# Kernel optimization log

Measured on AMD Instinct MI355X. Metric: run time of the kernel, lower is better.

Reference implementation:

```python
import jax, jax.numpy as jnp
import numpy as np
import math

FREQ_DIM = 161
OUTPUT_DIM = 4096
RNN_DIM = 128
EMBED_DIM = 32


def conv2d(x, w, b, stride):
    # x: (B, Cin, H, W), w: (Cout, Cin, kh, kw)
    out = jax.lax.conv_general_dilated(x, w, window_strides=stride, padding='VALID',
                                       dimension_numbers=('NCHW', 'OIHW', 'NCHW'))
    return out + b[None, :, None, None]


def gru_seq(x, w_ih, w_hh, b_ih, b_hh, h0):
    # x: (B, T, D); PyTorch GRU gate order: r, z, n
    B, T, D = x.shape
    H = h0.shape[-1]
    xg = jnp.einsum('btd,gd->btg', x, w_ih) + b_ih  # (B, T, 3H)

    def step(h, xg_t):
        hg = h @ w_hh.T + b_hh
        xr, xz, xn = jnp.split(xg_t, 3, axis=-1)
        hr, hz, hn = jnp.split(hg, 3, axis=-1)
        r = jax.nn.sigmoid(xr + hr)
        z = jax.nn.sigmoid(xz + hz)
        n = jnp.tanh(xn + r * hn)
        h_new = (1 - z) * n + z * h
        return h_new, h_new

    _, hs = jax.lax.scan(step, h0, jnp.swapaxes(xg, 0, 1))
    return jnp.swapaxes(hs, 0, 1)  # (B, T, H)


def gru_cell(ix, h, w_ih, w_hh, b_ih, b_hh):
    xg = ix @ w_ih.T + b_ih
    hg = h @ w_hh.T + b_hh
    xr, xz, xn = jnp.split(xg, 3, axis=-1)
    hr, hz, hn = jnp.split(hg, 3, axis=-1)
    r = jax.nn.sigmoid(xr + hr)
    z = jax.nn.sigmoid(xz + hz)
    n = jnp.tanh(xn + r * hn)
    return (1 - z) * n + z * h


def attend(eh, dhx):
    # eh: (B, T, H), dhx: (B, H)
    scores = jnp.einsum('bth,bh->bt', eh, dhx)
    a = jax.nn.softmax(scores, axis=-1)
    return jnp.einsum('bth,bt->bh', eh, a)


def setup_inputs() -> dict:
    key = jax.random.key(0)
    ks = jax.random.split(key, 16)

    def rn(k, shape, fan_in):
        s = 1.0 / math.sqrt(fan_in)
        return jax.random.uniform(k, shape, jnp.float32, -s, s)

    B, T_audio, L = 32, 512, 128
    x = jax.random.normal(ks[0], (B, T_audio, FREQ_DIM), jnp.float32)
    y = jax.random.randint(ks[1], (B, L), 0, OUTPUT_DIM)

    conv_in = 544  # 17 * 32 after two convs on freq dim 161
    params = {
        'conv1_w': rn(ks[2], (32, 1, 5, 32), 1 * 5 * 32),
        'conv1_b': rn(ks[3], (32,), 1 * 5 * 32),
        'conv2_w': rn(ks[4], (32, 32, 5, 32), 32 * 5 * 32),
        'conv2_b': rn(ks[5], (32,), 32 * 5 * 32),
        'rnn_w_ih': rn(ks[6], (3 * RNN_DIM, conv_in), RNN_DIM),
        'rnn_w_hh': rn(ks[7], (3 * RNN_DIM, RNN_DIM), RNN_DIM),
        'rnn_b_ih': rn(ks[8], (3 * RNN_DIM,), RNN_DIM),
        'rnn_b_hh': rn(ks[9], (3 * RNN_DIM,), RNN_DIM),
        'emb': jax.random.normal(ks[10], (OUTPUT_DIM, EMBED_DIM), jnp.float32),
        'dec_w_ih': rn(ks[11], (3 * RNN_DIM, EMBED_DIM), RNN_DIM),
        'dec_w_hh': rn(ks[12], (3 * RNN_DIM, RNN_DIM), RNN_DIM),
        'dec_b_ih': rn(ks[13], (3 * RNN_DIM,), RNN_DIM),
        'dec_b_hh': rn(ks[14], (3 * RNN_DIM,), RNN_DIM),
        'fc_w': rn(ks[15], (OUTPUT_DIM, RNN_DIM), RNN_DIM),
        'fc_b': rn(jax.random.fold_in(key, 99), (OUTPUT_DIM,), RNN_DIM),
        'h_init': jnp.zeros((1, RNN_DIM), jnp.float32),
    }
    return {'x': x, 'y': y, **params}


def forward(x, y, conv1_w, conv1_b, conv2_w, conv2_b,
            rnn_w_ih, rnn_w_hh, rnn_b_ih, rnn_b_hh,
            emb, dec_w_ih, dec_w_hh, dec_b_ih, dec_b_hh,
            fc_w, fc_b, h_init):
    B = x.shape[0]
    h = x[:, None, :, :]  # (B, 1, T, F)
    h = jax.nn.relu(conv2d(h, conv1_w, conv1_b, (2, 2)))
    h = jax.nn.relu(conv2d(h, conv2_w, conv2_b, (2, 2)))  # (B, 32, t, f)
    h = jnp.transpose(h, (0, 2, 3, 1))  # (B, t, f, c)
    b, t, f, c = h.shape
    h = h.reshape(b, t, f * c)
    eh = gru_seq(h, rnn_w_ih, rnn_w_hh, rnn_b_ih, rnn_b_hh,
                 jnp.zeros((b, RNN_DIM), h.dtype))  # (B, t, 128)

    inputs = emb[y[:, :-1]]  # (B, L-1, 32)
    hx = jnp.broadcast_to(h_init, (B, RNN_DIM))
    hx = hx + attend(eh, hx)

    def step(hx, ix):
        hx = gru_cell(ix, hx, dec_w_ih, dec_w_hh, dec_b_ih, dec_b_hh)
        hx = hx + attend(eh, hx)
        return hx, hx

    _, outs = jax.lax.scan(step, hx, jnp.swapaxes(inputs, 0, 1))
    out = jnp.concatenate([hx[:, None, :], jnp.swapaxes(outs, 0, 1)], axis=1)  # (B, L, 128)
    logits = jnp.einsum('btd,od->bto', out, fc_w) + fc_b
    return logits


def reference(x, y, conv1_w, conv1_b, conv2_w, conv2_b,
              rnn_w_ih, rnn_w_hh, rnn_b_ih, rnn_b_hh,
              emb, dec_w_ih, dec_w_hh, dec_b_ih, dec_b_hh,
              fc_w, fc_b, h_init):
    return forward(x, y, conv1_w, conv1_b, conv2_w, conv2_b,
                   rnn_w_ih, rnn_w_hh, rnn_b_ih, rnn_b_hh,
                   emb, dec_w_ih, dec_w_hh, dec_b_ih, dec_b_hh,
                   fc_w, fc_b, h_init)
```

## Files before the change

### kernel.cpp

```cpp
#include <hip/hip_runtime.h>
#include <stdint.h>

typedef unsigned short u16;
typedef uint32_t u32;

typedef __bf16 bf16x8 __attribute__((ext_vector_type(8)));
typedef float f32x4 __attribute__((ext_vector_type(4)));
typedef _Float16 h2v __attribute__((ext_vector_type(2)));

union B8 { uint4 q; u32 u[4]; bf16x8 v; };

__device__ __forceinline__ u16 f2bf(float f) {
  u32 u = __float_as_uint(f);
  u32 r = (u + 0x7fffu + ((u >> 16) & 1u)) >> 16;
  return (u16)r;
}
__device__ __forceinline__ u16 f2h(float f) {
  union { _Float16 h; u16 u; } v; v.h = (_Float16)f; return v.u;
}
__device__ __forceinline__ float dot2h(u32 a, u32 b, float c) {
  union U { u32 u; h2v v; } A, B; A.u = a; B.u = b;
  return __builtin_amdgcn_fdot2(A.v, B.v, c, false);
}
__device__ __forceinline__ float sigf(float x) { return 1.f / (1.f + __expf(-x)); }
__device__ __forceinline__ float tanhf_fast(float x) {
  x = fminf(fmaxf(x, -15.f), 15.f);
  float e = __expf(2.f * x);
  return (e - 1.f) / (e + 1.f);
}

__device__ __forceinline__ void prep_one(int e,
    const float* rnn_w_hh, const float* dec_w_hh, const float* conv1_w,
    const float* conv2_w, const float* rnn_w_ih, const float* dec_w_ih,
    const float* fc_w, const float* emb, const int* y,
    u32* wT2e, u32* wT2d, u16* w1b, u16* w2b, u16* wihb, u16* dwihb,
    u16* fcwb, u16* adec)
{
  const int S0 = 24576, S1 = 24576, S2 = 5120, S3 = 163840, S4 = 208896,
            S5 = 12288, S6 = 524288, S7 = 130048;
  if (e < S0) { int g = e >> 6, k2 = e & 63;
    wT2e[e] = (u32)f2h(rnn_w_hh[g*128 + 2*k2]) | ((u32)f2h(rnn_w_hh[g*128 + 2*k2 + 1]) << 16);
    return; }
  e -= S0;
  if (e < S1) { int g = e >> 6, k2 = e & 63;
    wT2d[e] = (u32)f2h(dec_w_hh[g*128 + 2*k2]) | ((u32)f2h(dec_w_hh[g*128 + 2*k2 + 1]) << 16);
    return; }
  e -= S1;
  if (e < S2) { int kh = e >> 10, c = (e >> 5) & 31, kw = e & 31;
    w1b[e] = f2bf(conv1_w[c*160 + kh*32 + kw]); return; }
  e -= S2;
  if (e < S3) { int kt = e >> 10, c = (e >> 5) & 31, kw = e & 31;
    int ic = kt / 5, kh = kt - ic * 5;
    w2b[e] = f2bf(conv2_w[((c*32 + ic)*5 + kh)*32 + kw]); return; }
  e -= S3;
  if (e < S4) { wihb[e] = f2bf(rnn_w_ih[e]); return; }
  e -= S4;
  if (e < S5) { dwihb[e] = f2bf(dec_w_ih[e]); return; }
  e -= S5;
  if (e < S6) { fcwb[e] = f2bf(fc_w[e]); return; }
  e -= S6;
  if (e < S7) { int m = e >> 5, k = e & 31;
    int b = m / 127, t = m - b * 127;
    adec[e] = f2bf(emb[y[b*128 + t]*32 + k]); return; }
}

__global__ __launch_bounds__(256) void prep_k(
    const float* rnn_w_hh, const float* dec_w_hh, const float* conv1_w,
    const float* conv2_w, const float* rnn_w_ih, const float* dec_w_ih,
    const float* fc_w, const float* emb, const int* y,
    u32* wT2e, u32* wT2d, u16* w1b, u16* w2b, u16* wihb, u16* dwihb,
    u16* fcwb, u16* adec)
{
  int e0 = blockIdx.x * 256 + threadIdx.x;
  #pragma unroll
  for (int it = 0; it < 4; it++) {
    int e = e0 + it * 273408;
    if (e < 1093632)
      prep_one(e, rnn_w_hh, dec_w_hh, conv1_w, conv2_w, rnn_w_ih, dec_w_ih,
               fc_w, emb, y, wT2e, wT2d, w1b, w2b, wihb, dwihb, fcwb, adec);
  }
}

__global__ __launch_bounds__(256) void conv1_k(const float* x, const u16* w1b,
                                               const float* c1b, u16* in1b)
{
  __shared__ __align__(16) u16 slab[35 * 162];
  __shared__ __align__(16) u16 wl[5120];
  int b = blockIdx.x >> 4;
  int oh0 = (blockIdx.x & 15) * 16;
  int ih0 = oh0 * 2;
  for (int e = threadIdx.x; e < 35 * 161; e += 256) {
    int r = e / 161, iw = e - r * 161;
    int ih = ih0 + r;
    float v = (ih < 512) ? x[(b*512 + ih)*161 + iw] : 0.f;
    slab[r*162 + iw] = f2bf(v);
  }
  for (int e = threadIdx.x; e < 5120; e += 256) wl[e] = w1b[e];
  __syncthreads();
  int lane = threadIdx.x & 63, wid = threadIdx.x >> 6;
  int lrow = lane & 15, lk = (lane >> 4) * 8;
  B8 bw[5][2];
  #pragma unroll
  for (int kt = 0; kt < 5; kt++)
    #pragma unroll
    for (int ct = 0; ct < 2; ct++)
      bw[kt][ct].q = *(const uint4*)&wl[(kt*32 + ct*16 + lrow)*32 + lk];
  float bias0 = c1b[lrow], bias1 = c1b[16 + lrow];
  for (int mt = wid; mt < 65; mt += 4) {
    int m = mt * 16 + lrow;
    int ohl = m / 65, ow = m - ohl * 65;
    int ro = ohl * 324 + ow * 2 + lk;
    f32x4 a0, a1;
    #pragma unroll
    for (int i = 0; i < 4; i++) { a0[i] = 0.f; a1[i] = 0.f; }
    #pragma unroll
    for (int kt = 0; kt < 5; kt++) {
      B8 af;
      const u32* p = (const u32*)&slab[ro + kt * 162];
      af.u[0] = p[0]; af.u[1] = p[1]; af.u[2] = p[2]; af.u[3] = p[3];
      a0 = __builtin_amdgcn_mfma_f32_16x16x32_bf16(af.v, bw[kt][0].v, a0, 0, 0, 0);
      a1 = __builtin_amdgcn_mfma_f32_16x16x32_bf16(af.v, bw[kt][1].v, a1, 0, 0, 0);
    }
    int rb = mt * 16 + (lane >> 4) * 4;
    #pragma unroll
    for (int i = 0; i < 4; i++) {
      int mr = rb + i;
      int ohl2 = mr / 65, ow2 = mr - ohl2 * 65;
      int oh = oh0 + ohl2;
      if (oh < 254) {
        float v0 = fmaxf(a0[i] + bias0, 0.f);
        float v1 = fmaxf(a1[i] + bias1, 0.f);
        in1b[((b*32 + lrow)*254 + oh)*72 + ow2] = f2bf(v0);
        in1b[((b*32 + 16 + lrow)*254 + oh)*72 + ow2] = f2bf(v1);
      }
    }
  }
}

__global__ __launch_bounds__(256) void conv2_k(const u16* in1b, const u16* w2b,
                                               const float* c2b, u16* hbf)
{
  extern __shared__ char smem[];
  u16* slab = (u16*)smem;
  u16* wl = (u16*)(smem + 50688);
  int b = blockIdx.x >> 5;
  int tile = blockIdx.x & 31;
  int oh0 = tile * 4;
  int ih0 = oh0 * 2;
  for (int q = threadIdx.x; q < 3168; q += 256) {
    int ic = q / 99;
    int rem = q - ic * 99;
    int r = rem / 9, j = rem - r * 9;
    int ih = ih0 + r;
    uint4 v = make_uint4(0u, 0u, 0u, 0u);
    if (ih < 254) v = *(const uint4*)&in1b[(((b*32 + ic)*254 + ih)*72) + j*8];
    *(uint4*)&slab[(ic*11 + r)*72 + j*8] = v;
  }
  int lane = threadIdx.x & 63, wid = threadIdx.x >> 6;
  int lrow = lane & 15, lk = (lane >> 4) * 8;
  int ohl_[2], ow_[2];
  #pragma unroll
  for (int q = 0; q < 2; q++) {
    int mt = (q == 1) ? 4 : wid;
    int m = mt * 16 + lrow;
    if (m > 67) m = 0;
    ohl_[q] = m / 17; ow_[q] = m - ohl_[q] * 17;
  }
  f32x4 acc[2][2];
  #pragma unroll
  for (int q = 0; q < 2; q++)
    #pragma unroll
    for (int ct = 0; ct < 2; ct++)
      #pragma unroll
      for (int i = 0; i < 4; i++) acc[q][ct][i] = 0.f;

  for (int ph = 0; ph < 16; ph++) {
    __syncthreads();
    {
      const uint4* s4 = (const uint4*)&w2b[ph * 10240];
      uint4* d4 = (uint4*)wl;
      for (int q = threadIdx.x; q < 1280; q += 256) d4[q] = s4[q];
    }
    __syncthreads();
    for (int ktl = 0; ktl < 10; ktl++) {
      int ktg = ph * 10 + ktl;
      int ic = ktg / 5, kh = ktg - ic * 5;
      B8 fb0, fb1;
      fb0.q = *(const uint4*)&wl[(ktl*32 + lrow)*32 + lk];
      fb1.q = *(const uint4*)&wl[(ktl*32 + 16 + lrow)*32 + lk];
      int base = (ic * 11 + kh) * 72 + lk;
      #pragma unroll
      for (int q = 0; q < 2; q++) {
        if (q == 1 && wid != 0) break;
        B8 af;
        const u32* p = (const u32*)&slab[base + ohl_[q] * 144 + ow_[q] * 2];
        af.u[0] = p[0]; af.u[1] = p[1]; af.u[2] = p[2]; af.u[3] = p[3];
        acc[q][0] = __builtin_amdgcn_mfma_f32_16x16x32_bf16(af.v, fb0.v, acc[q][0], 0, 0, 0);
        acc[q][1] = __builtin_amdgcn_mfma_f32_16x16x32_bf16(af.v, fb1.v, acc[q][1], 0, 0, 0);
      }
    }
  }
  #pragma unroll
  for (int q = 0; q < 2; q++) {
    if (q == 1 && wid != 0) break;
    int mt = (q == 1) ? 4 : wid;
    int rb = mt * 16 + (lane >> 4) * 4;
    #pragma unroll
    for (int ct = 0; ct < 2; ct++) {
      int c = ct * 16 + lrow;
      float bias = c2b[c];
      #pragma unroll
      for (int i = 0; i < 4; i++) {
        int mr = rb + i;
        if (mr < 68) {
          int ohl = mr / 17, ow = mr - ohl * 17;
          int oh = oh0 + ohl;
          if (oh < 125) {
            float v = fmaxf(acc[q][ct][i] + bias, 0.f);
            hbf[(b*125 + oh)*544 + ow*32 + c] = f2bf(v);
          }
        }
      }
    }
  }
}

__global__ __launch_bounds__(256) void gemm_k(const u16* A, const u16* Bw,
                                              const float* bias, float* C,
                                              int M, int N, int K)
{
  __shared__ __align__(16) u16 As[64 * 32];
  __shared__ __align__(16) u16 Bs[64 * 32];
  int m0 = blockIdx.x * 64, n0 = blockIdx.y * 64;
  int tid = threadIdx.x;
  int lane = tid & 63, wid = tid >> 6;
  int lrow = lane & 15, lk = (lane >> 4) * 8;
  int sr = tid >> 2, sc8 = (tid & 3) * 8;
  f32x4 acc[4];
  #pragma unroll
  for (int nt = 0; nt < 4; nt++)
    #pragma unroll
    for (int i = 0; i < 4; i++) acc[nt][i] = 0.f;
  int nkt = K >> 5;
  for (int kt = 0; kt < nkt; kt++) {
    __syncthreads();
    uint4 va = make_uint4(0u, 0u, 0u, 0u);
    int arow = m0 + sr;
    if (arow < M) va = *(const uint4*)&A[arow * K + kt * 32 + sc8];
    *(uint4*)&As[sr * 32 + sc8] = va;
    uint4 vb = *(const uint4*)&Bw[(n0 + sr) * K + kt * 32 + sc8];
    *(uint4*)&Bs[sr * 32 + sc8] = vb;
    __syncthreads();
    B8 af; af.q = *(const uint4*)&As[(wid * 16 + lrow) * 32 + lk];
    #pragma unroll
    for (int nt = 0; nt < 4; nt++) {
      B8 bb; bb.q = *(const uint4*)&Bs[(nt * 16 + lrow) * 32 + lk];
      acc[nt] = __builtin_amdgcn_mfma_f32_16x16x32_bf16(af.v, bb.v, acc[nt], 0, 0, 0);
    }
  }
  #pragma unroll
  for (int nt = 0; nt < 4; nt++) {
    int col = n0 + nt * 16 + lrow;
    float bv = bias[col];
    #pragma unroll
    for (int i = 0; i < 4; i++) {
      int row = m0 + wid * 16 + (lane >> 4) * 4 + i;
      if (row < M) C[row * N + col] = acc[nt][i] + bv;
    }
  }
}

__global__ __launch_bounds__(256) void fc_k(const u16* A, const u16* Bw,
                                            const float* bias, float* C)
{
  __shared__ __align__(16) u16 As[128 * 32];
  __shared__ __align__(16) u16 Bs[64 * 32];
  int m0 = blockIdx.x * 128, n0 = blockIdx.y * 64;
  int tid = threadIdx.x;
  int lane = tid & 63, wid = tid >> 6;
  int lrow = lane & 15, lk = (lane >> 4) * 8;
  f32x4 acc[2][4];
  #pragma unroll
  for (int mq = 0; mq < 2; mq++)
    #pragma unroll
    for (int nt = 0; nt < 4; nt++)
      #pragma unroll
      for (int i = 0; i < 4; i++) acc[mq][nt][i] = 0.f;
  #pragma unroll
  for (int kt = 0; kt < 4; kt++) {
    __syncthreads();
    #pragma unroll
    for (int i = tid; i < 512; i += 256) {
      int row = i >> 2, q = i & 3;
      *(uint4*)&As[row * 32 + q * 8] = *(const uint4*)&A[(m0 + row) * 128 + kt * 32 + q * 8];
    }
    {
      int row = tid >> 2, q = tid & 3;
      *(uint4*)&Bs[row * 32 + q * 8] = *(const uint4*)&Bw[(n0 + row) * 128 + kt * 32 + q * 8];
    }
    __syncthreads();
    B8 bb[4];
    #pragma unroll
    for (int nt = 0; nt < 4; nt++) bb[nt].q = *(const uint4*)&Bs[(nt * 16 + lrow) * 32 + lk];
    #pragma unroll
    for (int mq = 0; mq < 2; mq++) {
      B8 af; af.q = *(const uint4*)&As[((wid * 2 + mq) * 16 + lrow) * 32 + lk];
      #pragma unroll
      for (int nt = 0; nt < 4; nt++)
        acc[mq][nt] = __builtin_amdgcn_mfma_f32_16x16x32_bf16(af.v, bb[nt].v, acc[mq][nt], 0, 0, 0);
    }
  }
  #pragma unroll
  for (int nt = 0; nt < 4; nt++) {
    int col = n0 + nt * 16 + lrow;
    float bv = bias[col];
    #pragma unroll
    for (int mq = 0; mq < 2; mq++)
      #pragma unroll
      for (int i = 0; i < 4; i++) {
        int row = m0 + (wid * 2 + mq) * 16 + (lane >> 4) * 4 + i;
        C[(size_t)row * 4096 + col] = acc[mq][nt][i] + bv;
      }
  }
}

__global__ __launch_bounds__(1024, 1) void enc_k(const u32* wT2, const float* xg,
                                                 const float* bhh_g, u16* ehk, u16* eht)
{
  __shared__ __align__(16) u32 hp[2][2][64];
  __shared__ float hg[2][1152];
  int tid = threadIdx.x;
  int g = tid >> 9, tb = tid & 511, kh = tb >> 7, t = tb & 127;
  int b = blockIdx.x * 2 + g;
  u32 w0[16], w1[16], w2[16];
  {
    const uint4* p0 = (const uint4*)(wT2 + (size_t)t * 64 + kh * 16);
    const uint4* p1 = (const uint4*)(wT2 + (size_t)(128 + t) * 64 + kh * 16);
    const uint4* p2 = (const uint4*)(wT2 + (size_t)(256 + t) * 64 + kh * 16);
    #pragma unroll
    for (int j = 0; j < 4; j++) {
      uint4 q0 = p0[j]; w0[4*j] = q0.x; w0[4*j+1] = q0.y; w0[4*j+2] = q0.z; w0[4*j+3] = q0.w;
      uint4 q1 = p1[j]; w1[4*j] = q1.x; w1[4*j+1] = q1.y; w1[4*j+2] = q1.z; w1[4*j+3] = q1.w;
      uint4 q2 = p2[j]; w2[4*j] = q2.x; w2[4*j+1] = q2.y; w2[4*j+2] = q2.z; w2[4*j+3] = q2.w;
    }
  }
  float b0 = 0.f, b1 = 0.f, b2 = 0.f, xr0 = 0.f, xr1 = 0.f, xr2 = 0.f, hreg = 0.f;
  if (kh == 0) {
    b0 = bhh_g[t]; b1 = bhh_g[128 + t]; b2 = bhh_g[256 + t];
    const float* xp = &xg[(size_t)b * 125 * 384];
    xr0 = xp[t]; xr1 = xp[128 + t]; xr2 = xp[256 + t];
    ((u16*)&hp[g][0][0])[t] = 0;
  }
  __syncthreads();
  for (int tt = 0; tt < 125; tt++) {
    const u32* hb = &hp[g][tt & 1][kh * 16];
    float r0 = 0.f, r1 = 0.f, z0 = 0.f, z1 = 0.f, n0 = 0.f, n1 = 0.f;
    #pragma unroll
    for (int j = 0; j < 4; j++) {
      uint4 hv = *(const uint4*)&hb[4*j];
      r0 = dot2h(w0[4*j+0], hv.x, r0); r1 = dot2h(w0[4*j+1], hv.y, r1);
      r0 = dot2h(w0[4*j+2], hv.z, r0); r1 = dot2h(w0[4*j+3], hv.w, r1);
      z0 = dot2h(w1[4*j+0], hv.x, z0); z1 = dot2h(w1[4*j+1], hv.y, z1);
      z0 = dot2h(w1[4*j+2], hv.z, z0); z1 = dot2h(w1[4*j+3], hv.w, z1);
      n0 = dot2h(w2[4*j+0], hv.x, n0); n1 = dot2h(w2[4*j+1], hv.y, n1);
      n0 = dot2h(w2[4*j+2], hv.z, n0); n1 = dot2h(w2[4*j+3], hv.w, n1);
    }
    if (kh) {
      float* hh = &hg[g][(kh - 1) * 384];
      hh[t] = r0 + r1; hh[128 + t] = z0 + z1; hh[256 + t] = n0 + n1;
    }
    __syncthreads();
    if (kh == 0) {
      const float* hh = &hg[g][0];
      float pr = r0 + r1 + hh[t] + hh[384 + t] + hh[768 + t];
      float pz = z0 + z1 + hh[128 + t] + hh[512 + t] + hh[896 + t];
      float pn = n0 + n1 + hh[256 + t] + hh[640 + t] + hh[1024 + t];
      float r = sigf(xr0 + pr + b0);
      float z = sigf(xr1 + pz + b1);
      float n = tanhf_fast(xr2 + r * (pn + b2));
      hreg = (1.f - z) * n + z * hreg;
      u16 hv = f2h(hreg);
      ((u16*)&hp[g][(tt & 1) ^ 1][0])[t] = hv;
      ehk[((size_t)(b*64 + (t >> 1)) * 125 + tt) * 2 + (t & 1)] = hv;
      eht[((size_t)(b*128 + t)) * 128 + tt] = hv;
      if (tt + 1 < 125) {
        const float* xq = &xg[((size_t)b * 125 + tt + 1) * 384];
        xr0 = xq[t]; xr1 = xq[128 + t]; xr2 = xq[256 + t];
      }
    }
    __syncthreads();
  }
  if (kh == 0) {
    size_t rb = ((size_t)(b*128 + t)) * 128;
    eht[rb + 125] = 0; eht[rb + 126] = 0; eht[rb + 127] = 0;
  }
}

__global__ __launch_bounds__(1024, 1) void dec_k(const u32* wT2, const u32* ehk_g,
                                                 const u32* eht_g, const float* xgd,
                                                 const float* bhh_g, const float* h_init,
                                                 u16* outb)
{
  extern __shared__ char sm[];
  int tid = threadIdx.x;
  int g = tid >> 9, tb = tid & 511, kh = tb >> 7, t = tb & 127;
  int b = blockIdx.x * 2 + g;
  char* base = sm + (size_t)g * 41024;
  u32* elK   = (u32*)base;
  float* hgP = (float*)(base + 32000);
  float* sp  = (float*)(base + 36608);
  float* ctxB= (float*)(base + 38656);
  u16* hxA   = (u16*)(base + 40192);
  u16* hxB   = (u16*)(base + 40448);
  u16* scp   = (u16*)(base + 40704);
  float* red = (float*)(base + 40960);

  u32 w0[16], w1[16], w2[16];
  {
    const uint4* p0 = (const uint4*)(wT2 + (size_t)t * 64 + kh * 16);
    const uint4* p1 = (const uint4*)(wT2 + (size_t)(128 + t) * 64 + kh * 16);
    const uint4* p2 = (const uint4*)(wT2 + (size_t)(256 + t) * 64 + kh * 16);
    #pragma unroll
    for (int j = 0; j < 4; j++) {
      uint4 q0 = p0[j]; w0[4*j] = q0.x; w0[4*j+1] = q0.y; w0[4*j+2] = q0.z; w0[4*j+3] = q0.w;
      uint4 q1 = p1[j]; w1[4*j] = q1.x; w1[4*j+1] = q1.y; w1[4*j+2] = q1.z; w1[4*j+3] = q1.w;
      uint4 q2 = p2[j]; w2[4*j] = q2.x; w2[4*j+1] = q2.y; w2[4*j+2] = q2.z; w2[4*j+3] = q2.w;
    }
  }
  u32 rowr[16];
  {
    const uint4* rp = (const uint4*)(eht_g + (size_t)b * 8192 + (size_t)t * 64 + kh * 16);
    #pragma unroll
    for (int j = 0; j < 4; j++) {
      uint4 q = rp[j]; rowr[4*j] = q.x; rowr[4*j+1] = q.y; rowr[4*j+2] = q.z; rowr[4*j+3] = q.w;
    }
  }
  for (int e = tb; e < 8000; e += 512) elK[e] = ehk_g[(size_t)b * 8000 + e];
  float b0 = 0.f, b1 = 0.f, b2 = 0.f, xr0 = 0.f, xr1 = 0.f, xr2 = 0.f;
  float hxf = 0.f, hxg = 0.f;
  if (kh == 0) {
    b0 = bhh_g[t]; b1 = bhh_g[128 + t]; b2 = bhh_g[256 + t];
    hxf = h_init[t];
    const float* xp = &xgd[(size_t)b * 127 * 384];
    xr0 = xp[t]; xr1 = xp[128 + t]; xr2 = xp[256 + t];
  }
  __syncthreads();

  for (int step = 0; step < 128; step++) {
    if (step > 0) {
      const u32* hb = (const u32*)hxB + kh * 16;
      float r0 = 0.f, r1 = 0.f, z0 = 0.f, z1 = 0.f, n0 = 0.f, n1 = 0.f;
      #pragma unroll
      for (int j = 0; j < 4; j++) {
        uint4 hv = *(const uint4*)&hb[4*j];
        r0 = dot2h(w0[4*j+0], hv.x, r0); r1 = dot2h(w0[4*j+1], hv.y, r1);
        r0 = dot2h(w0[4*j+2], hv.z, r0); r1 = dot2h(w0[4*j+3], hv.w, r1);
        z0 = dot2h(w1[4*j+0], hv.x, z0); z1 = dot2h(w1[4*j+1], hv.y, z1);
        z0 = dot2h(w1[4*j+2], hv.z, z0); z1 = dot2h(w1[4*j+3], hv.w, z1);
        n0 = dot2h(w2[4*j+0], hv.x, n0); n1 = dot2h(w2[4*j+1], hv.y, n1);
        n0 = dot2h(w2[4*j+2], hv.z, n0); n1 = dot2h(w2[4*j+3], hv.w, n1);
      }
      if (kh) {
        float* hh = &hgP[(kh - 1) * 384];
        hh[t] = r0 + r1; hh[128 + t] = z0 + z1; hh[256 + t] = n0 + n1;
      }
      __syncthreads();
      if (kh == 0) {
        float pr = r0 + r1 + hgP[t] + hgP[384 + t] + hgP[768 + t];
        float pz = z0 + z1 + hgP[128 + t] + hgP[512 + t] + hgP[896 + t];
        float pn = n0 + n1 + hgP[256 + t] + hgP[640 + t] + hgP[1024 + t];
        float r = sigf(xr0 + pr + b0);
        float z = sigf(xr1 + pz + b1);
        float n = tanhf_fast(xr2 + r * (pn + b2));
        hxg = (1.f - z) * n + z * hxf;
        ((u16*)hxA)[t] = f2h(hxg);
        if (step < 127) {
          const float* xq = &xgd[((size_t)b * 127 + step) * 384];
          xr0 = xq[t]; xr1 = xq[128 + t]; xr2 = xq[256 + t];
        }
      }
      __syncthreads();
    } else {
      if (kh == 0) { hxg = hxf; ((u16*)hxA)[t] = f2h(hxg); }
      __syncthreads();
    }
    {
      float s0 = 0.f, s1 = 0.f;
      const u32* ek = &elK[(kh * 16) * 125];
      const u32* hxA4 = (const u32*)hxA;
      #pragma unroll
      for (int j = 0; j < 4; j++) {
        uint4 aw = *(const uint4*)&hxA4[kh * 16 + 4*j];
        s0 = dot2h(ek[(4*j+0)*125 + t], aw.x, s0);
        s1 = dot2h(ek[(4*j+1)*125 + t], aw.y, s1);
        s0 = dot2h(ek[(4*j+2)*125 + t], aw.z, s0);
        s1 = dot2h(ek[(4*j+3)*125 + t], aw.w, s1);
      }
      sp[kh * 128 + t] = s0 + s1;
    }
    __syncthreads();
    if (kh == 0) {
      float s = (t < 125) ? (sp[t] + sp[128 + t] + sp[256 + t] + sp[384 + t]) : -1e30f;
      float mw = s;
      #pragma unroll
      for (int o = 32; o > 0; o >>= 1) mw = fmaxf(mw, __shfl_xor(mw, o));
      float ev = (t < 125) ? __expf(s - mw) : 0.f;
      float sw = ev;
      #pragma unroll
      for (int o = 32; o > 0; o >>= 1) sw += __shfl_xor(sw, o);
      ((u16*)scp)[t] = f2h(ev);
      if ((t & 63) == 0) { int wv = t >> 6; red[wv*2] = mw; red[wv*2 + 1] = sw; }
    }
    __syncthreads();
    float m0r = red[0], S0r = red[1], m1r = red[2], S1r = red[3];
    float M = fmaxf(m0r, m1r);
    float f0 = __expf(m0r - M), f1 = __expf(m1r - M);
    float inv = 1.f / (f0 * S0r + f1 * S1r);
    float c0 = 0.f, c1 = 0.f;
    {
      const u32* scp4 = (const u32*)scp;
      #pragma unroll
      for (int j = 0; j < 4; j++) {
        uint4 sw4 = *(const uint4*)&scp4[kh * 16 + 4*j];
        c0 = dot2h(rowr[4*j+0], sw4.x, c0); c1 = dot2h(rowr[4*j+1], sw4.y, c1);
        c0 = dot2h(rowr[4*j+2], sw4.z, c0); c1 = dot2h(rowr[4*j+3], sw4.w, c1);
      }
    }
    if (kh) ctxB[(kh - 1) * 128 + t] = c0 + c1;
    __syncthreads();
    if (kh == 0) {
      float ctx = ((c0 + c1) + ctxB[t]) * f0 + (ctxB[128 + t] + ctxB[256 + t]) * f1;
      hxf = hxg + ctx * inv;
      outb[((size_t)(b * 128) + step) * 128 + t] = f2bf(hxf);
      ((u16*)hxB)[t] = f2h(hxf);
    }
    __syncthreads();
  }
}

extern "C" void kernel_launch(void* const* d_in, const int* in_sizes, int n_in,
                              void* d_out, int out_size, void* d_ws, size_t ws_size,
                              hipStream_t stream)
{
  const float* x        = (const float*)d_in[0];
  const int*   y        = (const int*)d_in[1];
  const float* conv1_w  = (const float*)d_in[2];
  const float* conv1_b  = (const float*)d_in[3];
  const float* conv2_w  = (const float*)d_in[4];
  const float* conv2_b  = (const float*)d_in[5];
  const float* rnn_w_ih = (const float*)d_in[6];
  const float* rnn_w_hh = (const float*)d_in[7];
  const float* rnn_b_ih = (const float*)d_in[8];
  const float* rnn_b_hh = (const float*)d_in[9];
  const float* emb      = (const float*)d_in[10];
  const float* dec_w_ih = (const float*)d_in[11];
  const float* dec_w_hh = (const float*)d_in[12];
  const float* dec_b_ih = (const float*)d_in[13];
  const float* dec_b_hh = (const float*)d_in[14];
  const float* fc_w     = (const float*)d_in[15];
  const float* fc_b     = (const float*)d_in[16];
  const float* h_init   = (const float*)d_in[17];
  float* logits = (float*)d_out;

  char* ws = (char*)d_ws;
  size_t off = 0;
  auto alloc = [&](size_t bytes) { char* p = ws + off; off = (off + bytes + 255) & ~(size_t)255; return p; };
  u16* in1b  = (u16*)alloc(37453824);
  u16* hbf   = (u16*)alloc(4352000);
  float* xge = (float*)alloc(6144000);
  u32* ehb_k = (u32*)alloc(1024000);
  u32* ehb_t = (u32*)alloc(1048576);
  float* xgd = (float*)alloc(6242304);
  u16* adec  = (u16*)alloc(260096);
  u16* outb  = (u16*)alloc(1048576);
  u32* wT2e  = (u32*)alloc(98304);
  u32* wT2d  = (u32*)alloc(98304);
  u16* w1b   = (u16*)alloc(10240);
  u16* w2b   = (u16*)alloc(327680);
  u16* wihb  = (u16*)alloc(417792);
  u16* dwihb = (u16*)alloc(24576);
  u16* fcwb  = (u16*)alloc(1048576);

  hipFuncSetAttribute((const void*)conv2_k, hipFuncAttributeMaxDynamicSharedMemorySize, 71168);
  hipFuncSetAttribute((const void*)dec_k,   hipFuncAttributeMaxDynamicSharedMemorySize, 82048);

  prep_k<<<1068, 256, 0, stream>>>(rnn_w_hh, dec_w_hh, conv1_w, conv2_w, rnn_w_ih,
                                   dec_w_ih, fc_w, emb, y,
                                   wT2e, wT2d, w1b, w2b, wihb, dwihb, fcwb, adec);
  conv1_k<<<512, 256, 0, stream>>>(x, w1b, conv1_b, in1b);
  conv2_k<<<1024, 256, 71168, stream>>>(in1b, w2b, conv2_b, hbf);
  gemm_k<<<dim3(63, 6), 256, 0, stream>>>(hbf, wihb, rnn_b_ih, xge, 4000, 384, 544);
  gemm_k<<<dim3(64, 6), 256, 0, stream>>>(adec, dwihb, dec_b_ih, xgd, 4064, 384, 32);
  enc_k<<<16, 1024, 0, stream>>>(wT2e, xge, rnn_b_hh, (u16*)ehb_k, (u16*)ehb_t);
  dec_k<<<16, 1024, 82048, stream>>>(wT2d, ehb_k, ehb_t, xgd, dec_b_hh, h_init, outb);
  fc_k<<<dim3(32, 64), 256, 0, stream>>>(outb, fcwb, fc_b, logits);
}
```

Measured before the change: 601.7 us.

## Stage recurrent input gates and outputs in LDS in 8-step chunks

In the encoder and decoder recurrent kernels, input-gate projections are now bulk-loaded into shared memory every 8 timesteps by all threads, replacing per-step scalar global loads on the critical path. Hidden-state outputs are likewise buffered in shared memory and written out as coalesced 32-bit chunks every 8 steps, replacing scattered 16-bit stores. The aim is to take global memory latency off the serial recurrence. In exchange the kernels use more shared memory, and every eighth step carries a burst of global traffic.

```diff
diff --git a/kernel.cpp b/kernel.cpp
--- a/kernel.cpp
+++ b/kernel.cpp
@@ -325,13 +325,16 @@
 }
 
 __global__ __launch_bounds__(1024, 1) void enc_k(const u32* wT2, const float* xg,
-                                                 const float* bhh_g, u16* ehk, u16* eht)
+                                                 const float* bhh_g, u32* ehk, u32* eht)
 {
   __shared__ __align__(16) u32 hp[2][2][64];
   __shared__ float hg[2][1152];
+  __shared__ __align__(16) float xgL[2][3072];
+  __shared__ __align__(16) u32 ehkC[2][512];
+  __shared__ __align__(16) u32 ehtC[2][512];
   int tid = threadIdx.x;
   int g = tid >> 9, tb = tid & 511, kh = tb >> 7, t = tb & 127;
-  int b = blockIdx.x * 2 + g;
+  int bg = blockIdx.x * 2 + g;
   u32 w0[16], w1[16], w2[16];
   {
     const uint4* p0 = (const uint4*)(wT2 + (size_t)t * 64 + kh * 16);
@@ -344,15 +347,29 @@
       uint4 q2 = p2[j]; w2[4*j] = q2.x; w2[4*j+1] = q2.y; w2[4*j+2] = q2.z; w2[4*j+3] = q2.w;
     }
   }
-  float b0 = 0.f, b1 = 0.f, b2 = 0.f, xr0 = 0.f, xr1 = 0.f, xr2 = 0.f, hreg = 0.f;
+  float b0 = 0.f, b1 = 0.f, b2 = 0.f, hreg = 0.f;
   if (kh == 0) {
     b0 = bhh_g[t]; b1 = bhh_g[128 + t]; b2 = bhh_g[256 + t];
-    const float* xp = &xg[(size_t)b * 125 * 384];
-    xr0 = xp[t]; xr1 = xp[128 + t]; xr2 = xp[256 + t];
     ((u16*)&hp[g][0][0])[t] = 0;
   }
   __syncthreads();
   for (int tt = 0; tt < 125; tt++) {
+    if (tt && (tt & 7) == 0) {
+      int tb0 = tt - 8;
+      { int k2 = tb >> 3, i = tb & 7;
+        ehk[(size_t)(bg*64 + k2)*125 + tb0 + i] = ehkC[g][k2*8 + i]; }
+      { int t2 = tb >> 2, i = tb & 3;
+        eht[(size_t)(bg*128 + t2)*64 + (tb0 >> 1) + i] = ehtC[g][t2*4 + i]; }
+    }
+    if ((tt & 7) == 0) {
+      #pragma unroll
+      for (int i = 0; i < 6; i++) {
+        int idx = tb + i * 512;
+        int r = idx / 384, col = idx - r * 384;
+        int gr = tt + r;
+        xgL[g][idx] = (gr < 125) ? xg[((size_t)bg * 125 + gr) * 384 + col] : 0.f;
+      }
+    }
     const u32* hb = &hp[g][tt & 1][kh * 16];
     float r0 = 0.f, r1 = 0.f, z0 = 0.f, z1 = 0.f, n0 = 0.f, n1 = 0.f;
     #pragma unroll
@@ -372,27 +389,31 @@
     __syncthreads();
     if (kh == 0) {
       const float* hh = &hg[g][0];
+      const float* xr = &xgL[g][(tt & 7) * 384];
       float pr = r0 + r1 + hh[t] + hh[384 + t] + hh[768 + t];
       float pz = z0 + z1 + hh[128 + t] + hh[512 + t] + hh[896 + t];
       float pn = n0 + n1 + hh[256 + t] + hh[640 + t] + hh[1024 + t];
-      float r = sigf(xr0 + pr + b0);
-      float z = sigf(xr1 + pz + b1);
-      float n = tanhf_fast(xr2 + r * (pn + b2));
+      float r = sigf(xr[t] + pr + b0);
+      float z = sigf(xr[128 + t] + pz + b1);
+      float n = tanhf_fast(xr[256 + t] + r * (pn + b2));
       hreg = (1.f - z) * n + z * hreg;
       u16 hv = f2h(hreg);
       ((u16*)&hp[g][(tt & 1) ^ 1][0])[t] = hv;
-      ehk[((size_t)(b*64 + (t >> 1)) * 125 + tt) * 2 + (t & 1)] = hv;
-      eht[((size_t)(b*128 + t)) * 128 + tt] = hv;
-      if (tt + 1 < 125) {
-        const float* xq = &xg[((size_t)b * 125 + tt + 1) * 384];
-        xr0 = xq[t]; xr1 = xq[128 + t]; xr2 = xq[256 + t];
-      }
+      ((u16*)&ehkC[g][0])[(t >> 1) * 16 + (tt & 7) * 2 + (t & 1)] = hv;
+      ((u16*)&ehtC[g][0])[t * 8 + (tt & 7)] = hv;
     }
     __syncthreads();
   }
   if (kh == 0) {
-    size_t rb = ((size_t)(b*128 + t)) * 128;
-    eht[rb + 125] = 0; eht[rb + 126] = 0; eht[rb + 127] = 0;
+    u16* ec = (u16*)&ehtC[g][0];
+    ec[t*8 + 5] = 0; ec[t*8 + 6] = 0; ec[t*8 + 7] = 0;
+  }
+  __syncthreads();
+  {
+    { int k2 = tb >> 3, i = tb & 7, ttg = 120 + i;
+      if (ttg < 125) ehk[(size_t)(bg*64 + k2)*125 + ttg] = ehkC[g][k2*8 + i]; }
+    { int t2 = tb >> 2, i = tb & 3;
+      eht[(size_t)(bg*128 + t2)*64 + 60 + i] = ehtC[g][t2*4 + i]; }
   }
 }
 
@@ -405,15 +426,17 @@
   int tid = threadIdx.x;
   int g = tid >> 9, tb = tid & 511, kh = tb >> 7, t = tb & 127;
   int b = blockIdx.x * 2 + g;
-  char* base = sm + (size_t)g * 41024;
-  u32* elK   = (u32*)base;
-  float* hgP = (float*)(base + 32000);
-  float* sp  = (float*)(base + 36608);
-  float* ctxB= (float*)(base + 38656);
-  u16* hxA   = (u16*)(base + 40192);
-  u16* hxB   = (u16*)(base + 40448);
-  u16* scp   = (u16*)(base + 40704);
-  float* red = (float*)(base + 40960);
+  char* base = sm + (size_t)g * 55360;
+  u32* elK    = (u32*)base;
+  float* hgP  = (float*)(base + 32000);
+  float* sp   = (float*)(base + 36608);
+  float* ctxB = (float*)(base + 38656);
+  u16* hxA    = (u16*)(base + 40192);
+  u16* hxB    = (u16*)(base + 40448);
+  u16* scp    = (u16*)(base + 40704);
+  float* red  = (float*)(base + 40960);
+  float* xgdL = (float*)(base + 41024);
+  u32* outbL  = (u32*)(base + 53312);
 
   u32 w0[16], w1[16], w2[16];
   {
@@ -436,17 +459,18 @@
     }
   }
   for (int e = tb; e < 8000; e += 512) elK[e] = ehk_g[(size_t)b * 8000 + e];
-  float b0 = 0.f, b1 = 0.f, b2 = 0.f, xr0 = 0.f, xr1 = 0.f, xr2 = 0.f;
+  float b0 = 0.f, b1 = 0.f, b2 = 0.f;
   float hxf = 0.f, hxg = 0.f;
   if (kh == 0) {
     b0 = bhh_g[t]; b1 = bhh_g[128 + t]; b2 = bhh_g[256 + t];
     hxf = h_init[t];
-    const float* xp = &xgd[(size_t)b * 127 * 384];
-    xr0 = xp[t]; xr1 = xp[128 + t]; xr2 = xp[256 + t];
   }
   __syncthreads();
 
   for (int step = 0; step < 128; step++) {
+    if (step && (step & 7) == 0) {
+      ((u32*)outb)[(size_t)(b * 128 + step - 8) * 64 + tb] = outbL[tb];
+    }
     if (step > 0) {
       const u32* hb = (const u32*)hxB + kh * 16;
       float r0 = 0.f, r1 = 0.f, z0 = 0.f, z1 = 0.f, n0 = 0.f, n1 = 0.f;
@@ -466,23 +490,29 @@
       }
       __syncthreads();
       if (kh == 0) {
+        const float* xr = &xgdL[((step - 1) & 7) * 384];
         float pr = r0 + r1 + hgP[t] + hgP[384 + t] + hgP[768 + t];
         float pz = z0 + z1 + hgP[128 + t] + hgP[512 + t] + hgP[896 + t];
         float pn = n0 + n1 + hgP[256 + t] + hgP[640 + t] + hgP[1024 + t];
-        float r = sigf(xr0 + pr + b0);
-        float z = sigf(xr1 + pz + b1);
-        float n = tanhf_fast(xr2 + r * (pn + b2));
+        float r = sigf(xr[t] + pr + b0);
+        float z = sigf(xr[128 + t] + pz + b1);
+        float n = tanhf_fast(xr[256 + t] + r * (pn + b2));
         hxg = (1.f - z) * n + z * hxf;
         ((u16*)hxA)[t] = f2h(hxg);
-        if (step < 127) {
-          const float* xq = &xgd[((size_t)b * 127 + step) * 384];
-          xr0 = xq[t]; xr1 = xq[128 + t]; xr2 = xq[256 + t];
-        }
       }
       __syncthreads();
     } else {
       if (kh == 0) { hxg = hxf; ((u16*)hxA)[t] = f2h(hxg); }
       __syncthreads();
+    }
+    if ((step & 7) == 0) {
+      #pragma unroll
+      for (int i = 0; i < 6; i++) {
+        int idx = tb + i * 512;
+        int r = idx / 384, col = idx - r * 384;
+        int gr = step + r;
+        if (gr < 127) xgdL[idx] = xgd[((size_t)b * 127 + gr) * 384 + col];
+      }
     }
     {
       float s0 = 0.f, s1 = 0.f;
@@ -531,11 +561,12 @@
     if (kh == 0) {
       float ctx = ((c0 + c1) + ctxB[t]) * f0 + (ctxB[128 + t] + ctxB[256 + t]) * f1;
       hxf = hxg + ctx * inv;
-      outb[((size_t)(b * 128) + step) * 128 + t] = f2bf(hxf);
+      ((u16*)outbL)[(step & 7) * 128 + t] = f2bf(hxf);
       ((u16*)hxB)[t] = f2h(hxf);
     }
     __syncthreads();
   }
+  ((u32*)outb)[(size_t)(b * 128 + 120) * 64 + tb] = outbL[tb];
 }
 
 extern "C" void kernel_launch(void* const* d_in, const int* in_sizes, int n_in,
@@ -582,7 +613,7 @@
   u16* fcwb  = (u16*)alloc(1048576);
 
   hipFuncSetAttribute((const void*)conv2_k, hipFuncAttributeMaxDynamicSharedMemorySize, 71168);
-  hipFuncSetAttribute((const void*)dec_k,   hipFuncAttributeMaxDynamicSharedMemorySize, 82048);
+  hipFuncSetAttribute((const void*)dec_k,   hipFuncAttributeMaxDynamicSharedMemorySize, 110720);
 
   prep_k<<<1068, 256, 0, stream>>>(rnn_w_hh, dec_w_hh, conv1_w, conv2_w, rnn_w_ih,
                                    dec_w_ih, fc_w, emb, y,
@@ -591,7 +622,7 @@
   conv2_k<<<1024, 256, 71168, stream>>>(in1b, w2b, conv2_b, hbf);
   gemm_k<<<dim3(63, 6), 256, 0, stream>>>(hbf, wihb, rnn_b_ih, xge, 4000, 384, 544);
   gemm_k<<<dim3(64, 6), 256, 0, stream>>>(adec, dwihb, dec_b_ih, xgd, 4064, 384, 32);
-  enc_k<<<16, 1024, 0, stream>>>(wT2e, xge, rnn_b_hh, (u16*)ehb_k, (u16*)ehb_t);
-  dec_k<<<16, 1024, 82048, stream>>>(wT2d, ehb_k, ehb_t, xgd, dec_b_hh, h_init, outb);
+  enc_k<<<16, 1024, 0, stream>>>(wT2e, xge, rnn_b_hh, ehb_k, ehb_t);
+  dec_k<<<16, 1024, 110720, stream>>>(wT2d, ehb_k, ehb_t, xgd, dec_b_hh, h_init, outb);
   fc_k<<<dim3(32, 64), 256, 0, stream>>>(outb, fcwb, fc_b, logits);
 }
```

After: 669.6 us. 1.11x slower.
